# Kernel tuning notes

Hardware: AMD Instinct MI355X
Metric: run time of the kernel (lower is better)

## Reference

```python
import jax, jax.numpy as jnp
import numpy as np
from jax import lax

K = 7            # cfg.network.PSROI_BINS == pool_size
FEAT_STRIDE = 16
LAMDA = 0.1
D_PER_BIN = 8    # feature channels per position-sensitive bin -> C = K*K*8 = 392


def _bilinear(feat, y, x, extra_idx):
    """Bilinearly sample feat[H,W,...] at float coords (y,x); extra_idx are
    integer index arrays (broadcast to y.shape) selecting trailing feat axes."""
    H, W = feat.shape[0], feat.shape[1]
    y0f = jnp.floor(y); x0f = jnp.floor(x)
    wy = (y - y0f)[..., None]
    wx = (x - x0f)[..., None]
    y0 = jnp.clip(y0f.astype(jnp.int32), 0, H - 1)
    y1 = jnp.clip(y0f.astype(jnp.int32) + 1, 0, H - 1)
    x0 = jnp.clip(x0f.astype(jnp.int32), 0, W - 1)
    x1 = jnp.clip(x0f.astype(jnp.int32) + 1, 0, W - 1)
    def g(yi, xi):
        return feat[(yi, xi) + extra_idx]
    return ((1 - wy) * (1 - wx) * g(y0, x0) + (1 - wy) * wx * g(y0, x1)
            + wy * (1 - wx) * g(y1, x0) + wy * wx * g(y1, x1))


def ps_roi(f, rois, k, feat_stride, offsets=None):
    """Position-sensitive RoI pooling. f: [H,W,C] with C = k*k*D (bin-major
    channel layout). rois: [N,5] (batch, x1, y1, x2, y2) in image coords.
    offsets (optional): [N, k*k, G, 2] per-bin, per-channel-group (x,y) shifts
    in image coords. Returns [N, D, k, k]."""
    H, W, C = f.shape
    N = rois.shape[0]
    kk = k * k
    D = C // kk
    x1 = rois[:, 1] / feat_stride
    y1 = rois[:, 2] / feat_stride
    x2 = (rois[:, 3] + 1.0) / feat_stride
    y2 = (rois[:, 4] + 1.0) / feat_stride
    bw = (x2 - x1) / k  # [N]
    bh = (y2 - y1) / k
    jj = jnp.tile(jnp.arange(k, dtype=f.dtype), k)     # bin = i*k + j
    ii = jnp.repeat(jnp.arange(k, dtype=f.dtype), k)
    cx = x1[:, None] + (jj + 0.5) * bw[:, None]        # [N, kk] bin centers
    cy = y1[:, None] + (ii + 0.5) * bh[:, None]
    bins = jnp.arange(kk, dtype=jnp.int32)
    if offsets is None:
        feat = f.reshape(H, W, kk, D)
        b = jnp.broadcast_to(bins, (N, kk))
        vals = _bilinear(feat, cy, cx, (b,))           # [N, kk, D]
    else:
        G = offsets.shape[2]
        cxg = cx[:, :, None] + offsets[..., 0] / feat_stride  # [N, kk, G]
        cyg = cy[:, :, None] + offsets[..., 1] / feat_stride
        feat = f.reshape(H, W, kk, G, D // G)
        b = jnp.broadcast_to(bins[None, :, None], (N, kk, G))
        g = jnp.broadcast_to(jnp.arange(G, dtype=jnp.int32)[None, None, :], (N, kk, G))
        vals = _bilinear(feat, cyg, cxg, (b, g))       # [N, kk, G, D//G]
        vals = vals.reshape(N, kk, D)
    return jnp.transpose(vals.reshape(N, k, k, D), (0, 3, 1, 2))  # [N, D, k, k]


def setup_inputs():
    key = jax.random.key(0)
    kf, kw, k1, k2 = jax.random.split(key, 4)
    H = W = 128
    C = K * K * D_PER_BIN
    N = 2048
    features = jax.random.normal(kf, (1, H, W, C), jnp.float32)
    conv_w = jax.random.normal(kw, (3, 3, C, 2 * 4 * K * K), jnp.float32) * 0.01
    img = float(H * FEAT_STRIDE)
    xy1 = jax.random.uniform(k1, (N, 2), minval=0.0, maxval=img * 0.6)
    wh = jax.random.uniform(k2, (N, 2), minval=32.0, maxval=img * 0.4)
    xy2 = jnp.minimum(xy1 + wh, img - 1.0)
    rois = jnp.concatenate([jnp.zeros((N, 1)), xy1[:, :1], xy1[:, 1:], xy2[:, :1], xy2[:, 1:]], axis=1).astype(jnp.float32)
    return {"features": features, "rois": rois, "conv_w": conv_w}


def reference(features, rois, conv_w):
    # offset branch: 3x3 conv (no bias) -> PS-RoI pool -> scale by lamda*roi size
    offset_map = lax.conv_general_dilated(features, conv_w, (1, 1), 'SAME',
                                          dimension_numbers=('NHWC', 'HWIO', 'NHWC'))
    off = ps_roi(offset_map[0], rois, K, FEAT_STRIDE)          # [N, 8, K, K]
    N = off.shape[0]
    off = off.reshape(N, -1, 2, K, K)                          # [N, 4, 2, K, K]
    off = jnp.transpose(off, (2, 3, 4, 1, 0))                  # [2, K, K, 4, N]
    roi_w = rois[:, 3] - rois[:, 1] + 1.0
    roi_h = rois[:, 4] - rois[:, 2] + 1.0
    off = jnp.stack((off[0] * roi_w * LAMDA, off[1] * roi_h * LAMDA), axis=0)
    off = jnp.transpose(off, (4, 1, 2, 3, 0))                  # [N, K, K, 4, 2]
    off = off.reshape(N, K * K, -1, 2)                         # [N, kk, 4, 2]
    # deformable PS-RoI pooling of the features with predicted offsets
    return ps_roi(features[0], rois, K, FEAT_STRIDE, offsets=off)  # [N, 8, K, K]
```

## Files before the change

### kernel.cpp

```cpp
#include <hip/hip_runtime.h>
#include <cstddef>
#include <cstdint>

#define HH    128
#define WW    128
#define CC    392
#define NPIX  (HH*WW)
#define NROI  2048
#define PSK   7
#define NBIN  49
#define LAMDA 0.1f

#define CPAD      448
#define HPAD      130
#define NPADCO    512
#define SEGSTRIDE (9*CPAD)
#define BKK       64

#define FBM 64
#define FBN 64
#define FBK 32

typedef _Float16 half8   __attribute__((ext_vector_type(8)));
typedef float    floatx4 __attribute__((ext_vector_type(4)));

__device__ __forceinline__ void async_ld16(const _Float16* g, _Float16* l) {
  __builtin_amdgcn_global_load_lds((const __attribute__((address_space(1))) void*)g,
                                   (__attribute__((address_space(3))) void*)l,
                                   16, 0, 0);
}

__global__ __launch_bounds__(256)
void conv_f_kernel(const float* __restrict__ F, _Float16* __restrict__ Fh) {
  const int idx = blockIdx.x * 256 + threadIdx.x;
  const int total = HPAD * HPAD * (CPAD / 8);
  if (idx >= total) return;
  const int p  = idx / (CPAD / 8);
  const int cg = idx - p * (CPAD / 8);
  const int c  = cg * 8;
  const int py = p / HPAD;
  const int px = p - py * HPAD;
  half8 h;
#pragma unroll
  for (int i = 0; i < 8; ++i) h[i] = (_Float16)0.f;
  if (py >= 1 && py <= HH && px >= 1 && px <= WW && c < CC) {
    const float* src = F + ((size_t)(py - 1) * WW + (px - 1)) * CC + c;
    const float4 v0 = *(const float4*)src;
    const float4 v1 = *(const float4*)(src + 4);
    h[0] = (_Float16)v0.x; h[1] = (_Float16)v0.y;
    h[2] = (_Float16)v0.z; h[3] = (_Float16)v0.w;
    h[4] = (_Float16)v1.x; h[5] = (_Float16)v1.y;
    h[6] = (_Float16)v1.z; h[7] = (_Float16)v1.w;
  }
  *(half8*)(Fh + (size_t)p * CPAD + c) = h;
}

__global__ __launch_bounds__(256)
void conv_w_kernel(const float* __restrict__ Wt, _Float16* __restrict__ Bth) {
  __shared__ float tile[32][33];
  const int bid = blockIdx.x;
  const int seg = bid / (14 * 16);
  const int rem = bid - seg * (14 * 16);
  const int cit = rem / 16;
  const int cot = rem - cit * 16;
  const int ci0 = cit * 32, co0 = cot * 32;
  const int t = threadIdx.x;
#pragma unroll
  for (int i = 0; i < 4; ++i) {
    const int idx = t + i * 256;
    const int lr = idx >> 5;
    const int lc = idx & 31;
    const int ci = ci0 + lr, co = co0 + lc;
    float v = 0.f;
    if (ci < CC && co < CC) v = Wt[((size_t)seg * CC + ci) * CC + co];
    tile[lr][lc] = v;
  }
  __syncthreads();
#pragma unroll
  for (int i = 0; i < 4; ++i) {
    const int idx = t + i * 256;
    const int lr = idx >> 5;
    const int lc = idx & 31;
    Bth[(size_t)(co0 + lr) * SEGSTRIDE + seg * CPAD + ci0 + lc] = (_Float16)tile[lc][lr];
  }
}

__global__ __launch_bounds__(256, 2)
void conv_mfma_kernel(const _Float16* __restrict__ Fh, const _Float16* __restrict__ Bth,
                      _Float16* __restrict__ OM) {
  __shared__ __align__(16) _Float16 As[128 * BKK];
  __shared__ __align__(16) _Float16 Bs[128 * BKK];

  const int t = threadIdx.x;
  const int L = t & 63;
  const int w = t >> 6;
  const int row0 = blockIdx.x * 128;
  const int col0 = blockIdx.y * 128;

  const int srow = L >> 3;
  const int kofs = ((L & 7) ^ srow) * 8;

  const int ya = row0 >> 7;
  const int nbase = col0 + w * 32 + srow;

  const int wm = (w >> 1) * 64;
  const int wn = (w & 1) * 64;
  const int fr = L & 15;
  const int quad = L >> 4;
  const int pg0 = (quad ^ (fr & 7)) * 8;
  const int pg1 = ((4 + quad) ^ (fr & 7)) * 8;

  floatx4 acc[4][4];
#pragma unroll
  for (int i = 0; i < 4; ++i)
#pragma unroll
    for (int j = 0; j < 4; ++j) {
      floatx4 z = {0.f, 0.f, 0.f, 0.f};
      acc[i][j] = z;
    }

  for (int seg = 0; seg < 9; ++seg) {
    const int dy = seg / 3 - 1;
    const int dx = seg - (seg / 3) * 3 - 1;
    const int fy = ya + 1 + dy;
    const _Float16* gArow = Fh + ((size_t)fy * HPAD + (1 + dx)) * CPAD + kofs;
    const _Float16* gB = Bth + (size_t)nbase * SEGSTRIDE + seg * CPAD + kofs;

    for (int it = 0; it < 7; ++it) {
      const int cb = it * BKK;
#pragma unroll
      for (int j = 0; j < 4; ++j) {
        const int xr = w * 32 + j * 8 + srow;
        async_ld16(gArow + (size_t)xr * CPAD + cb, &As[(w * 32 + j * 8) * BKK]);
      }
#pragma unroll
      for (int j = 0; j < 4; ++j) {
        async_ld16(gB + (size_t)(j * 8) * SEGSTRIDE + cb, &Bs[(w * 32 + j * 8) * BKK]);
      }
      __syncthreads();

      half8 a0[4], a1[4], b0[4], b1[4];
#pragma unroll
      for (int mt = 0; mt < 4; ++mt) {
        const int rb = (wm + mt * 16 + fr) * BKK;
        a0[mt] = *(const half8*)(&As[rb + pg0]);
        a1[mt] = *(const half8*)(&As[rb + pg1]);
      }
#pragma unroll
      for (int nt = 0; nt < 4; ++nt) {
        const int rb = (wn + nt * 16 + fr) * BKK;
        b0[nt] = *(const half8*)(&Bs[rb + pg0]);
        b1[nt] = *(const half8*)(&Bs[rb + pg1]);
      }
#pragma unroll
      for (int mt = 0; mt < 4; ++mt)
#pragma unroll
        for (int nt = 0; nt < 4; ++nt)
          acc[mt][nt] = __builtin_amdgcn_mfma_f32_16x16x32_f16(a0[mt], b0[nt], acc[mt][nt], 0, 0, 0);
#pragma unroll
      for (int mt = 0; mt < 4; ++mt)
#pragma unroll
        for (int nt = 0; nt < 4; ++nt)
          acc[mt][nt] = __builtin_amdgcn_mfma_f32_16x16x32_f16(a1[mt], b1[nt], acc[mt][nt], 0, 0, 0);
      __syncthreads();
    }
  }

#pragma unroll
  for (int mt = 0; mt < 4; ++mt) {
    const int rbase = row0 + wm + mt * 16 + quad * 4;
#pragma unroll
    for (int nt = 0; nt < 4; ++nt) {
      const int col = col0 + wn + nt * 16 + fr;
      if (col < CC) {
#pragma unroll
        for (int r = 0; r < 4; ++r)
          OM[(size_t)(rbase + r) * CC + col] = (_Float16)acc[mt][nt][r];
      }
    }
  }
}

__global__ __launch_bounds__(256)
void conv3x3_kernel(const float* __restrict__ F, const float* __restrict__ Wt,
                    float* __restrict__ OM) {
  __shared__ float Asf[FBK][FBM + 4];
  __shared__ float Bsf[FBK][FBN + 4];

  const int t = threadIdx.x;
  const int ty = t >> 4;
  const int tx = t & 15;
  const int row0 = blockIdx.x * FBM;
  const int col0 = blockIdx.y * FBN;

  float acc[4][4];
#pragma unroll
  for (int i = 0; i < 4; ++i)
#pragma unroll
    for (int j = 0; j < 4; ++j) acc[i][j] = 0.f;

  for (int kc = 0; kc < 117; ++kc) {
    const int seg   = kc / 13;
    const int cbase = (kc - seg * 13) * FBK;
    const int dy    = seg / 3 - 1;
    const int dx    = seg - (seg / 3) * 3 - 1;

#pragma unroll
    for (int rep = 0; rep < (FBM * FBK) / 256; ++rep) {
      const int idx = t + rep * 256;
      const int r  = idx >> 5;
      const int lk = idx & 31;
      const int m  = row0 + r;
      const int y  = m >> 7, x = m & 127;
      const int yy = y + dy, xx = x + dx;
      const int ci = cbase + lk;
      float v = 0.f;
      if ((unsigned)yy < HH && (unsigned)xx < WW && ci < CC)
        v = F[((size_t)(yy * WW + xx)) * CC + ci];
      Asf[lk][r] = v;
    }
#pragma unroll
    for (int rep = 0; rep < (FBK * FBN) / 256; ++rep) {
      const int idx = t + rep * 256;
      const int lk  = idx >> 6;
      const int nn  = idx & 63;
      const int ci  = cbase + lk;
      const int col = col0 + nn;
      float v = 0.f;
      if (ci < CC && col < CC)
        v = Wt[((size_t)(seg * CC + ci)) * CC + col];
      Bsf[lk][nn] = v;
    }
    __syncthreads();

#pragma unroll
    for (int lk = 0; lk < FBK; ++lk) {
      const float4 a4 = *(const float4*)(&Asf[lk][ty * 4]);
      const float4 b4 = *(const float4*)(&Bsf[lk][tx * 4]);
      const float av[4] = {a4.x, a4.y, a4.z, a4.w};
      const float bv[4] = {b4.x, b4.y, b4.z, b4.w};
#pragma unroll
      for (int i = 0; i < 4; ++i)
#pragma unroll
        for (int j = 0; j < 4; ++j)
          acc[i][j] = fmaf(av[i], bv[j], acc[i][j]);
    }
    __syncthreads();
  }

  const int col = col0 + tx * 4;
  if (col < CC) {
#pragma unroll
    for (int i = 0; i < 4; ++i) {
      float4 v = make_float4(acc[i][0], acc[i][1], acc[i][2], acc[i][3]);
      *(float4*)(&OM[((size_t)(row0 + ty * 4 + i)) * CC + col]) = v;
    }
  }
}

__device__ __forceinline__ void bilin_setup(float y, float x,
                                            int& iy0, int& iy1, int& ix0, int& ix1,
                                            float& w00, float& w01, float& w10, float& w11) {
  const float y0f = floorf(y), x0f = floorf(x);
  const float wy = y - y0f, wx = x - x0f;
  const int a = (int)y0f, b = (int)x0f;
  iy0 = min(max(a, 0), HH - 1);
  iy1 = min(max(a + 1, 0), HH - 1);
  ix0 = min(max(b, 0), WW - 1);
  ix1 = min(max(b + 1, 0), WW - 1);
  w00 = (1.f - wy) * (1.f - wx);
  w01 = (1.f - wy) * wx;
  w10 = wy * (1.f - wx);
  w11 = wy * wx;
}

template <typename TOM>
__global__ __launch_bounds__(256)
void psroi_pool_kernel(const float* __restrict__ F, const float* __restrict__ R,
                       const TOM* __restrict__ OM, float* __restrict__ out) {
  const int tid = blockIdx.x * 256 + threadIdx.x;
  if (tid >= NROI * NBIN * 4) return;
  const int g  = tid & 3;
  const int nb = tid >> 2;
  const int n  = nb / NBIN;
  const int b  = nb - n * NBIN;
  const int bi = b / PSK;
  const int bj = b - bi * PSK;

  const float rx1 = R[n * 5 + 1], ry1 = R[n * 5 + 2];
  const float rx2 = R[n * 5 + 3], ry2 = R[n * 5 + 4];

  const float x1 = rx1 * (1.f / 16.f);
  const float y1 = ry1 * (1.f / 16.f);
  const float x2 = (rx2 + 1.f) * (1.f / 16.f);
  const float y2 = (ry2 + 1.f) * (1.f / 16.f);
  const float bw = (x2 - x1) * (1.f / 7.f);
  const float bh = (y2 - y1) * (1.f / 7.f);
  const float cx = x1 + ((float)bj + 0.5f) * bw;
  const float cy = y1 + ((float)bi + 0.5f) * bh;

  int iy0, iy1, ix0, ix1;
  float w00, w01, w10, w11;
  bilin_setup(cy, cx, iy0, iy1, ix0, ix1, w00, w01, w10, w11);

  const size_t c0 = (size_t)b * 8 + 2 * g;
  const size_t s00 = (size_t)(iy0 * WW + ix0) * CC + c0;
  const size_t s01 = (size_t)(iy0 * WW + ix1) * CC + c0;
  const size_t s10 = (size_t)(iy1 * WW + ix0) * CC + c0;
  const size_t s11 = (size_t)(iy1 * WW + ix1) * CC + c0;

  const float ox = w00 * (float)OM[s00]     + w01 * (float)OM[s01]
                 + w10 * (float)OM[s10]     + w11 * (float)OM[s11];
  const float oy = w00 * (float)OM[s00 + 1] + w01 * (float)OM[s01 + 1]
                 + w10 * (float)OM[s10 + 1] + w11 * (float)OM[s11 + 1];

  const float roiw = rx2 - rx1 + 1.f;
  const float roih = ry2 - ry1 + 1.f;
  const float sx = cx + ox * roiw * (LAMDA / 16.f);
  const float sy = cy + oy * roih * (LAMDA / 16.f);

  int jy0, jy1, jx0, jx1;
  float u00, u01, u10, u11;
  bilin_setup(sy, sx, jy0, jy1, jx0, jx1, u00, u01, u10, u11);

  const float2 q00 = *(const float2*)(F + (size_t)(jy0 * WW + jx0) * CC + c0);
  const float2 q01 = *(const float2*)(F + (size_t)(jy0 * WW + jx1) * CC + c0);
  const float2 q10 = *(const float2*)(F + (size_t)(jy1 * WW + jx0) * CC + c0);
  const float2 q11 = *(const float2*)(F + (size_t)(jy1 * WW + jx1) * CC + c0);

  const float v0 = u00 * q00.x + u01 * q01.x + u10 * q10.x + u11 * q11.x;
  const float v1 = u00 * q00.y + u01 * q01.y + u10 * q10.y + u11 * q11.y;

  out[((size_t)n * 8 + 2 * g + 0) * NBIN + b] = v0;
  out[((size_t)n * 8 + 2 * g + 1) * NBIN + b] = v1;
}

extern "C" void kernel_launch(void* const* d_in, const int* in_sizes, int n_in,
                              void* d_out, int out_size, void* d_ws, size_t ws_size,
                              hipStream_t stream) {
  const float* F  = (const float*)d_in[0];
  const float* R  = (const float*)d_in[1];
  const float* Wt = (const float*)d_in[2];
  float* out = (float*)d_out;

  const size_t omBytes  = (size_t)NPIX * CC * sizeof(_Float16);
  const size_t fhBytes  = (size_t)HPAD * HPAD * CPAD * sizeof(_Float16);
  const size_t bthBytes = (size_t)NPADCO * SEGSTRIDE * sizeof(_Float16);
  const size_t need = omBytes + fhBytes + bthBytes;

  const int totalPool = NROI * NBIN * 4;

  if (ws_size >= need) {
    _Float16* OM  = (_Float16*)d_ws;
    _Float16* Fh  = (_Float16*)((char*)d_ws + omBytes);
    _Float16* Bth = (_Float16*)((char*)d_ws + omBytes + fhBytes);

    const int fTotal = HPAD * HPAD * (CPAD / 8);
    conv_f_kernel<<<(fTotal + 255) / 256, 256, 0, stream>>>(F, Fh);
    conv_w_kernel<<<9 * 14 * 16, 256, 0, stream>>>(Wt, Bth);

    dim3 g(NPIX / 128, NPADCO / 128);
    conv_mfma_kernel<<<g, 256, 0, stream>>>(Fh, Bth, OM);

    psroi_pool_kernel<_Float16><<<(totalPool + 255) / 256, 256, 0, stream>>>(F, R, OM, out);
  } else {
    float* OM = (float*)d_ws;
    dim3 cgrid(NPIX / FBM, (CC + FBN - 1) / FBN);
    conv3x3_kernel<<<cgrid, 256, 0, stream>>>(F, Wt, OM);
    psroi_pool_kernel<float><<<(totalPool + 255) / 256, 256, 0, stream>>>(F, R, OM, out);
  }
}
```

Before: 166.4 us.

## Split conv GEMM K-dimension across two blocks and merge prep kernels

The 3x3 conv GEMM reduction (63 K-steps) is split in two halves via a z grid dimension, with each half writing a separate fp32 partial output map. The pooling kernel then sums the two partials when sampling offsets. The two prep kernels are fused into one launch, and the offset map is now stored in fp32 instead of fp16. This doubles the conv grid from 512 blocks to improve CU occupancy, at the cost of more workspace, twice the output-map write traffic and extra gathers in the pooling kernel.

Result: slower. 171.1 us (+2.8%).

```diff
diff --git a/kernel.cpp b/kernel.cpp
--- a/kernel.cpp
+++ b/kernel.cpp
@@ -16,6 +16,7 @@
 #define NPADCO    512
 #define SEGSTRIDE (9*CPAD)
 #define BKK       64
+#define NQ        63
 
 #define FBM 64
 #define FBN 64
@@ -30,64 +31,67 @@
                                    16, 0, 0);
 }
 
+#define FPREP ((HPAD * HPAD * (CPAD / 8) + 255) / 256)
+#define WPREP (9 * 14 * 16)
+
 __global__ __launch_bounds__(256)
-void conv_f_kernel(const float* __restrict__ F, _Float16* __restrict__ Fh) {
-  const int idx = blockIdx.x * 256 + threadIdx.x;
-  const int total = HPAD * HPAD * (CPAD / 8);
-  if (idx >= total) return;
-  const int p  = idx / (CPAD / 8);
-  const int cg = idx - p * (CPAD / 8);
-  const int c  = cg * 8;
-  const int py = p / HPAD;
-  const int px = p - py * HPAD;
-  half8 h;
-#pragma unroll
-  for (int i = 0; i < 8; ++i) h[i] = (_Float16)0.f;
-  if (py >= 1 && py <= HH && px >= 1 && px <= WW && c < CC) {
-    const float* src = F + ((size_t)(py - 1) * WW + (px - 1)) * CC + c;
-    const float4 v0 = *(const float4*)src;
-    const float4 v1 = *(const float4*)(src + 4);
-    h[0] = (_Float16)v0.x; h[1] = (_Float16)v0.y;
-    h[2] = (_Float16)v0.z; h[3] = (_Float16)v0.w;
-    h[4] = (_Float16)v1.x; h[5] = (_Float16)v1.y;
-    h[6] = (_Float16)v1.z; h[7] = (_Float16)v1.w;
-  }
-  *(half8*)(Fh + (size_t)p * CPAD + c) = h;
-}
-
-__global__ __launch_bounds__(256)
-void conv_w_kernel(const float* __restrict__ Wt, _Float16* __restrict__ Bth) {
+void prep_kernel(const float* __restrict__ F, const float* __restrict__ Wt,
+                 _Float16* __restrict__ Fh, _Float16* __restrict__ Bth) {
   __shared__ float tile[32][33];
-  const int bid = blockIdx.x;
-  const int seg = bid / (14 * 16);
-  const int rem = bid - seg * (14 * 16);
-  const int cit = rem / 16;
-  const int cot = rem - cit * 16;
-  const int ci0 = cit * 32, co0 = cot * 32;
   const int t = threadIdx.x;
-#pragma unroll
-  for (int i = 0; i < 4; ++i) {
-    const int idx = t + i * 256;
-    const int lr = idx >> 5;
-    const int lc = idx & 31;
-    const int ci = ci0 + lr, co = co0 + lc;
-    float v = 0.f;
-    if (ci < CC && co < CC) v = Wt[((size_t)seg * CC + ci) * CC + co];
-    tile[lr][lc] = v;
-  }
-  __syncthreads();
-#pragma unroll
-  for (int i = 0; i < 4; ++i) {
-    const int idx = t + i * 256;
-    const int lr = idx >> 5;
-    const int lc = idx & 31;
-    Bth[(size_t)(co0 + lr) * SEGSTRIDE + seg * CPAD + ci0 + lc] = (_Float16)tile[lc][lr];
+  if (blockIdx.x < FPREP) {
+    const int idx = blockIdx.x * 256 + t;
+    const int total = HPAD * HPAD * (CPAD / 8);
+    if (idx >= total) return;
+    const int p  = idx / (CPAD / 8);
+    const int cg = idx - p * (CPAD / 8);
+    const int c  = cg * 8;
+    const int py = p / HPAD;
+    const int px = p - py * HPAD;
+    half8 h;
+#pragma unroll
+    for (int i = 0; i < 8; ++i) h[i] = (_Float16)0.f;
+    if (py >= 1 && py <= HH && px >= 1 && px <= WW && c < CC) {
+      const float* src = F + ((size_t)(py - 1) * WW + (px - 1)) * CC + c;
+      const float4 v0 = *(const float4*)src;
+      const float4 v1 = *(const float4*)(src + 4);
+      h[0] = (_Float16)v0.x; h[1] = (_Float16)v0.y;
+      h[2] = (_Float16)v0.z; h[3] = (_Float16)v0.w;
+      h[4] = (_Float16)v1.x; h[5] = (_Float16)v1.y;
+      h[6] = (_Float16)v1.z; h[7] = (_Float16)v1.w;
+    }
+    *(half8*)(Fh + (size_t)p * CPAD + c) = h;
+  } else {
+    const int bid = blockIdx.x - FPREP;
+    const int seg = bid / (14 * 16);
+    const int rem = bid - seg * (14 * 16);
+    const int cit = rem / 16;
+    const int cot = rem - cit * 16;
+    const int ci0 = cit * 32, co0 = cot * 32;
+#pragma unroll
+    for (int i = 0; i < 4; ++i) {
+      const int idx = t + i * 256;
+      const int lr = idx >> 5;
+      const int lc = idx & 31;
+      const int ci = ci0 + lr, co = co0 + lc;
+      float v = 0.f;
+      if (ci < CC && co < CC) v = Wt[((size_t)seg * CC + ci) * CC + co];
+      tile[lr][lc] = v;
+    }
+    __syncthreads();
+#pragma unroll
+    for (int i = 0; i < 4; ++i) {
+      const int idx = t + i * 256;
+      const int lr = idx >> 5;
+      const int lc = idx & 31;
+      Bth[(size_t)(co0 + lr) * SEGSTRIDE + seg * CPAD + ci0 + lc] = (_Float16)tile[lc][lr];
+    }
   }
 }
 
 __global__ __launch_bounds__(256, 2)
 void conv_mfma_kernel(const _Float16* __restrict__ Fh, const _Float16* __restrict__ Bth,
-                      _Float16* __restrict__ OM) {
+                      float* __restrict__ OMbase, int span) {
   __shared__ __align__(16) _Float16 As[128 * BKK];
   __shared__ __align__(16) _Float16 Bs[128 * BKK];
 
@@ -96,6 +100,10 @@
   const int w = t >> 6;
   const int row0 = blockIdx.x * 128;
   const int col0 = blockIdx.y * 128;
+  const int kz   = blockIdx.z;
+  const int q0 = kz * span;
+  const int q1 = min(NQ, q0 + span);
+  float* __restrict__ OMp = OMbase + (size_t)kz * NPIX * CC;
 
   const int srow = L >> 3;
   const int kofs = ((L & 7) ^ srow) * 8;
@@ -119,51 +127,51 @@
       acc[i][j] = z;
     }
 
-  for (int seg = 0; seg < 9; ++seg) {
+  for (int q = q0; q < q1; ++q) {
+    const int seg = q / 7;
+    const int it  = q - seg * 7;
     const int dy = seg / 3 - 1;
     const int dx = seg - (seg / 3) * 3 - 1;
     const int fy = ya + 1 + dy;
-    const _Float16* gArow = Fh + ((size_t)fy * HPAD + (1 + dx)) * CPAD + kofs;
-    const _Float16* gB = Bth + (size_t)nbase * SEGSTRIDE + seg * CPAD + kofs;
-
-    for (int it = 0; it < 7; ++it) {
-      const int cb = it * BKK;
-#pragma unroll
-      for (int j = 0; j < 4; ++j) {
-        const int xr = w * 32 + j * 8 + srow;
-        async_ld16(gArow + (size_t)xr * CPAD + cb, &As[(w * 32 + j * 8) * BKK]);
-      }
-#pragma unroll
-      for (int j = 0; j < 4; ++j) {
-        async_ld16(gB + (size_t)(j * 8) * SEGSTRIDE + cb, &Bs[(w * 32 + j * 8) * BKK]);
-      }
-      __syncthreads();
-
-      half8 a0[4], a1[4], b0[4], b1[4];
-#pragma unroll
-      for (int mt = 0; mt < 4; ++mt) {
-        const int rb = (wm + mt * 16 + fr) * BKK;
-        a0[mt] = *(const half8*)(&As[rb + pg0]);
-        a1[mt] = *(const half8*)(&As[rb + pg1]);
-      }
-#pragma unroll
-      for (int nt = 0; nt < 4; ++nt) {
-        const int rb = (wn + nt * 16 + fr) * BKK;
-        b0[nt] = *(const half8*)(&Bs[rb + pg0]);
-        b1[nt] = *(const half8*)(&Bs[rb + pg1]);
-      }
-#pragma unroll
-      for (int mt = 0; mt < 4; ++mt)
-#pragma unroll
-        for (int nt = 0; nt < 4; ++nt)
-          acc[mt][nt] = __builtin_amdgcn_mfma_f32_16x16x32_f16(a0[mt], b0[nt], acc[mt][nt], 0, 0, 0);
-#pragma unroll
-      for (int mt = 0; mt < 4; ++mt)
-#pragma unroll
-        for (int nt = 0; nt < 4; ++nt)
-          acc[mt][nt] = __builtin_amdgcn_mfma_f32_16x16x32_f16(a1[mt], b1[nt], acc[mt][nt], 0, 0, 0);
-      __syncthreads();
-    }
+    const int cb = it * BKK;
+    const _Float16* gArow = Fh + ((size_t)fy * HPAD + (1 + dx)) * CPAD + kofs + cb;
+    const _Float16* gB = Bth + (size_t)nbase * SEGSTRIDE + seg * CPAD + kofs + cb;
+
+#pragma unroll
+    for (int j = 0; j < 4; ++j) {
+      const int xr = w * 32 + j * 8 + srow;
+      async_ld16(gArow + (size_t)xr * CPAD, &As[(w * 32 + j * 8) * BKK]);
+    }
+#pragma unroll
+    for (int j = 0; j < 4; ++j) {
+      async_ld16(gB + (size_t)(j * 8) * SEGSTRIDE, &Bs[(w * 32 + j * 8) * BKK]);
+    }
+    __syncthreads();
+
+    half8 a0[4], a1[4], b0[4], b1[4];
+#pragma unroll
+    for (int mt = 0; mt < 4; ++mt) {
+      const int rb = (wm + mt * 16 + fr) * BKK;
+      a0[mt] = *(const half8*)(&As[rb + pg0]);
+      a1[mt] = *(const half8*)(&As[rb + pg1]);
+    }
+#pragma unroll
+    for (int nt = 0; nt < 4; ++nt) {
+      const int rb = (wn + nt * 16 + fr) * BKK;
+      b0[nt] = *(const half8*)(&Bs[rb + pg0]);
+      b1[nt] = *(const half8*)(&Bs[rb + pg1]);
+    }
+#pragma unroll
+    for (int mt = 0; mt < 4; ++mt)
+#pragma unroll
+      for (int nt = 0; nt < 4; ++nt)
+        acc[mt][nt] = __builtin_amdgcn_mfma_f32_16x16x32_f16(a0[mt], b0[nt], acc[mt][nt], 0, 0, 0);
+#pragma unroll
+    for (int mt = 0; mt < 4; ++mt)
+#pragma unroll
+      for (int nt = 0; nt < 4; ++nt)
+        acc[mt][nt] = __builtin_amdgcn_mfma_f32_16x16x32_f16(a1[mt], b1[nt], acc[mt][nt], 0, 0, 0);
+    __syncthreads();
   }
 
 #pragma unroll
@@ -175,7 +183,7 @@
       if (col < CC) {
 #pragma unroll
         for (int r = 0; r < 4; ++r)
-          OM[(size_t)(rbase + r) * CC + col] = (_Float16)acc[mt][nt][r];
+          OMp[(size_t)(rbase + r) * CC + col] = acc[mt][nt][r];
       }
     }
   }
@@ -274,10 +282,10 @@
   w11 = wy * wx;
 }
 
-template <typename TOM>
 __global__ __launch_bounds__(256)
 void psroi_pool_kernel(const float* __restrict__ F, const float* __restrict__ R,
-                       const TOM* __restrict__ OM, float* __restrict__ out) {
+                       const float* __restrict__ OMa, const float* __restrict__ OMb,
+                       float* __restrict__ out, int dual) {
   const int tid = blockIdx.x * 256 + threadIdx.x;
   if (tid >= NROI * NBIN * 4) return;
   const int g  = tid & 3;
@@ -309,10 +317,22 @@
   const size_t s10 = (size_t)(iy1 * WW + ix0) * CC + c0;
   const size_t s11 = (size_t)(iy1 * WW + ix1) * CC + c0;
 
-  const float ox = w00 * (float)OM[s00]     + w01 * (float)OM[s01]
-                 + w10 * (float)OM[s10]     + w11 * (float)OM[s11];
-  const float oy = w00 * (float)OM[s00 + 1] + w01 * (float)OM[s01 + 1]
-                 + w10 * (float)OM[s10 + 1] + w11 * (float)OM[s11 + 1];
+  float2 m00 = *(const float2*)(OMa + s00);
+  float2 m01 = *(const float2*)(OMa + s01);
+  float2 m10 = *(const float2*)(OMa + s10);
+  float2 m11 = *(const float2*)(OMa + s11);
+  if (dual) {
+    const float2 e00 = *(const float2*)(OMb + s00);
+    const float2 e01 = *(const float2*)(OMb + s01);
+    const float2 e10 = *(const float2*)(OMb + s10);
+    const float2 e11 = *(const float2*)(OMb + s11);
+    m00.x += e00.x; m00.y += e00.y;
+    m01.x += e01.x; m01.y += e01.y;
+    m10.x += e10.x; m10.y += e10.y;
+    m11.x += e11.x; m11.y += e11.y;
+  }
+  const float ox = w00 * m00.x + w01 * m01.x + w10 * m10.x + w11 * m11.x;
+  const float oy = w00 * m00.y + w01 * m01.y + w10 * m10.y + w11 * m11.y;
 
   const float roiw = rx2 - rx1 + 1.f;
   const float roih = ry2 - ry1 + 1.f;
@@ -343,30 +363,37 @@
   const float* Wt = (const float*)d_in[2];
   float* out = (float*)d_out;
 
-  const size_t omBytes  = (size_t)NPIX * CC * sizeof(_Float16);
+  const size_t omBytes  = (size_t)NPIX * CC * sizeof(float);
   const size_t fhBytes  = (size_t)HPAD * HPAD * CPAD * sizeof(_Float16);
   const size_t bthBytes = (size_t)NPADCO * SEGSTRIDE * sizeof(_Float16);
-  const size_t need = omBytes + fhBytes + bthBytes;
+  const size_t needDual   = 2 * omBytes + fhBytes + bthBytes;
+  const size_t needSingle = omBytes + fhBytes + bthBytes;
 
   const int totalPool = NROI * NBIN * 4;
-
-  if (ws_size >= need) {
-    _Float16* OM  = (_Float16*)d_ws;
-    _Float16* Fh  = (_Float16*)((char*)d_ws + omBytes);
-    _Float16* Bth = (_Float16*)((char*)d_ws + omBytes + fhBytes);
-
-    const int fTotal = HPAD * HPAD * (CPAD / 8);
-    conv_f_kernel<<<(fTotal + 255) / 256, 256, 0, stream>>>(F, Fh);
-    conv_w_kernel<<<9 * 14 * 16, 256, 0, stream>>>(Wt, Bth);
-
-    dim3 g(NPIX / 128, NPADCO / 128);
-    conv_mfma_kernel<<<g, 256, 0, stream>>>(Fh, Bth, OM);
-
-    psroi_pool_kernel<_Float16><<<(totalPool + 255) / 256, 256, 0, stream>>>(F, R, OM, out);
+  const int poolGrid = (totalPool + 255) / 256;
+
+  if (ws_size >= needSingle) {
+    const int dual = (ws_size >= needDual) ? 1 : 0;
+    float* OMa = (float*)d_ws;
+    float* OMb = OMa + (size_t)NPIX * CC;
+    _Float16* Fh  = (_Float16*)((char*)d_ws + (dual ? 2 : 1) * omBytes);
+    _Float16* Bth = Fh + (size_t)HPAD * HPAD * CPAD;
+
+    prep_kernel<<<FPREP + WPREP, 256, 0, stream>>>(F, Wt, Fh, Bth);
+
+    if (dual) {
+      dim3 g(NPIX / 128, NPADCO / 128, 2);
+      conv_mfma_kernel<<<g, 256, 0, stream>>>(Fh, Bth, OMa, 32);
+    } else {
+      dim3 g(NPIX / 128, NPADCO / 128, 1);
+      conv_mfma_kernel<<<g, 256, 0, stream>>>(Fh, Bth, OMa, NQ);
+    }
+
+    psroi_pool_kernel<<<poolGrid, 256, 0, stream>>>(F, R, OMa, OMb, out, dual);
   } else {
-    float* OM = (float*)d_ws;
+    float* OMa = (float*)d_ws;
     dim3 cgrid(NPIX / FBM, (CC + FBN - 1) / FBN);
-    conv3x3_kernel<<<cgrid, 256, 0, stream>>>(F, Wt, OM);
-    psroi_pool_kernel<float><<<(totalPool + 255) / 256, 256, 0, stream>>>(F, R, OM, out);
-  }
-}
+    conv3x3_kernel<<<cgrid, 256, 0, stream>>>(F, Wt, OMa);
+    psroi_pool_kernel<<<poolGrid, 256, 0, stream>>>(F, R, OMa, OMa, out, 0);
+  }
+}
```

## Fuse prep, conv and pooling into one cooperative persistent kernel

Applied to the files above, without the earlier changes.

Replaces the four separate launches (feature cast, weight transpose, MFMA conv, PS-RoI pooling) with a single cooperative mega-kernel that uses grid-wide syncs between phases. The conv K-loop is flattened into one 63-step loop, and pooling now reads the padded fp16 feature copy with half2 loads instead of fp32 features. The aim is to remove launch gaps and halve the gather traffic in pooling. The risks are that only 512 of the 1024 blocks do conv work, that grid syncs cost time, and that the change drops the fallback path used when the workspace is too small.

New measurement: 165.9 us. About the same (-0.3%).

```diff
diff --git a/kernel.cpp b/kernel.cpp
--- a/kernel.cpp
+++ b/kernel.cpp
@@ -1,6 +1,9 @@
 #include <hip/hip_runtime.h>
+#include <hip/hip_cooperative_groups.h>
 #include <cstddef>
 #include <cstdint>
+
+namespace cg = cooperative_groups;
 
 #define HH    128
 #define WW    128
@@ -16,12 +19,17 @@
 #define NPADCO    512
 #define SEGSTRIDE (9*CPAD)
 #define BKK       64
-
-#define FBM 64
-#define FBN 64
-#define FBK 32
+#define NQ        63
+
+#define NBLK    1024
+#define NTHR    256
+#define GSTRIDE (NBLK*NTHR)
+#define FTOT    (HPAD*HPAD*(CPAD/8))
+#define WTILES  (9*14*16)
+#define POOLTOT (NROI*NBIN*4)
 
 typedef _Float16 half8   __attribute__((ext_vector_type(8)));
+typedef _Float16 half2v  __attribute__((ext_vector_type(2)));
 typedef float    floatx4 __attribute__((ext_vector_type(4)));
 
 __device__ __forceinline__ void async_ld16(const _Float16* g, _Float16* l) {
@@ -30,72 +38,72 @@
                                    16, 0, 0);
 }
 
-__global__ __launch_bounds__(256)
-void conv_f_kernel(const float* __restrict__ F, _Float16* __restrict__ Fh) {
-  const int idx = blockIdx.x * 256 + threadIdx.x;
-  const int total = HPAD * HPAD * (CPAD / 8);
-  if (idx >= total) return;
-  const int p  = idx / (CPAD / 8);
-  const int cg = idx - p * (CPAD / 8);
-  const int c  = cg * 8;
-  const int py = p / HPAD;
-  const int px = p - py * HPAD;
-  half8 h;
-#pragma unroll
-  for (int i = 0; i < 8; ++i) h[i] = (_Float16)0.f;
-  if (py >= 1 && py <= HH && px >= 1 && px <= WW && c < CC) {
-    const float* src = F + ((size_t)(py - 1) * WW + (px - 1)) * CC + c;
-    const float4 v0 = *(const float4*)src;
-    const float4 v1 = *(const float4*)(src + 4);
-    h[0] = (_Float16)v0.x; h[1] = (_Float16)v0.y;
-    h[2] = (_Float16)v0.z; h[3] = (_Float16)v0.w;
-    h[4] = (_Float16)v1.x; h[5] = (_Float16)v1.y;
-    h[6] = (_Float16)v1.z; h[7] = (_Float16)v1.w;
-  }
-  *(half8*)(Fh + (size_t)p * CPAD + c) = h;
-}
-
-__global__ __launch_bounds__(256)
-void conv_w_kernel(const float* __restrict__ Wt, _Float16* __restrict__ Bth) {
-  __shared__ float tile[32][33];
-  const int bid = blockIdx.x;
-  const int seg = bid / (14 * 16);
-  const int rem = bid - seg * (14 * 16);
-  const int cit = rem / 16;
-  const int cot = rem - cit * 16;
-  const int ci0 = cit * 32, co0 = cot * 32;
-  const int t = threadIdx.x;
-#pragma unroll
-  for (int i = 0; i < 4; ++i) {
-    const int idx = t + i * 256;
-    const int lr = idx >> 5;
-    const int lc = idx & 31;
-    const int ci = ci0 + lr, co = co0 + lc;
-    float v = 0.f;
-    if (ci < CC && co < CC) v = Wt[((size_t)seg * CC + ci) * CC + co];
-    tile[lr][lc] = v;
-  }
-  __syncthreads();
-#pragma unroll
-  for (int i = 0; i < 4; ++i) {
-    const int idx = t + i * 256;
-    const int lr = idx >> 5;
-    const int lc = idx & 31;
-    Bth[(size_t)(co0 + lr) * SEGSTRIDE + seg * CPAD + ci0 + lc] = (_Float16)tile[lc][lr];
-  }
-}
-
-__global__ __launch_bounds__(256, 2)
-void conv_mfma_kernel(const _Float16* __restrict__ Fh, const _Float16* __restrict__ Bth,
-                      _Float16* __restrict__ OM) {
-  __shared__ __align__(16) _Float16 As[128 * BKK];
-  __shared__ __align__(16) _Float16 Bs[128 * BKK];
-
-  const int t = threadIdx.x;
+__device__ __forceinline__ void prep_features(const float* __restrict__ F,
+                                              _Float16* __restrict__ Fh,
+                                              int gtid, int stride) {
+  for (int idx = gtid; idx < FTOT; idx += stride) {
+    const int p  = idx / (CPAD / 8);
+    const int cgi = idx - p * (CPAD / 8);
+    const int c  = cgi * 8;
+    const int py = p / HPAD;
+    const int px = p - py * HPAD;
+    half8 h;
+#pragma unroll
+    for (int i = 0; i < 8; ++i) h[i] = (_Float16)0.f;
+    if (py >= 1 && py <= HH && px >= 1 && px <= WW && c < CC) {
+      const float* src = F + ((size_t)(py - 1) * WW + (px - 1)) * CC + c;
+      const float4 v0 = *(const float4*)src;
+      const float4 v1 = *(const float4*)(src + 4);
+      h[0] = (_Float16)v0.x; h[1] = (_Float16)v0.y;
+      h[2] = (_Float16)v0.z; h[3] = (_Float16)v0.w;
+      h[4] = (_Float16)v1.x; h[5] = (_Float16)v1.y;
+      h[6] = (_Float16)v1.z; h[7] = (_Float16)v1.w;
+    }
+    *(half8*)(Fh + (size_t)p * CPAD + c) = h;
+  }
+}
+
+__device__ __forceinline__ void prep_weights(const float* __restrict__ Wt,
+                                             _Float16* __restrict__ Bth,
+                                             float (*tile)[33],
+                                             int bid, int t, int nblocks) {
+  for (int tl = bid; tl < WTILES; tl += nblocks) {
+    const int seg = tl / (14 * 16);
+    const int rem = tl - seg * (14 * 16);
+    const int cit = rem / 16;
+    const int cot = rem - cit * 16;
+    const int ci0 = cit * 32, co0 = cot * 32;
+    __syncthreads();
+#pragma unroll
+    for (int i = 0; i < 4; ++i) {
+      const int idx = t + i * 256;
+      const int lr = idx >> 5;
+      const int lc = idx & 31;
+      const int ci = ci0 + lr, co = co0 + lc;
+      float v = 0.f;
+      if (ci < CC && co < CC) v = Wt[((size_t)seg * CC + ci) * CC + co];
+      tile[lr][lc] = v;
+    }
+    __syncthreads();
+#pragma unroll
+    for (int i = 0; i < 4; ++i) {
+      const int idx = t + i * 256;
+      const int lr = idx >> 5;
+      const int lc = idx & 31;
+      Bth[(size_t)(co0 + lr) * SEGSTRIDE + seg * CPAD + ci0 + lc] = (_Float16)tile[lc][lr];
+    }
+  }
+}
+
+__device__ __forceinline__ void conv_phase(const _Float16* __restrict__ Fh,
+                                           const _Float16* __restrict__ Bth,
+                                           _Float16* __restrict__ OM,
+                                           _Float16* As, _Float16* Bs,
+                                           int cb, int t) {
   const int L = t & 63;
   const int w = t >> 6;
-  const int row0 = blockIdx.x * 128;
-  const int col0 = blockIdx.y * 128;
+  const int row0 = (cb & 127) * 128;
+  const int col0 = (cb >> 7) * 128;
 
   const int srow = L >> 3;
   const int kofs = ((L & 7) ^ srow) * 8;
@@ -119,51 +127,51 @@
       acc[i][j] = z;
     }
 
-  for (int seg = 0; seg < 9; ++seg) {
+  for (int q = 0; q < NQ; ++q) {
+    const int seg = q / 7;
+    const int it  = q - seg * 7;
     const int dy = seg / 3 - 1;
     const int dx = seg - (seg / 3) * 3 - 1;
     const int fy = ya + 1 + dy;
-    const _Float16* gArow = Fh + ((size_t)fy * HPAD + (1 + dx)) * CPAD + kofs;
-    const _Float16* gB = Bth + (size_t)nbase * SEGSTRIDE + seg * CPAD + kofs;
-
-    for (int it = 0; it < 7; ++it) {
-      const int cb = it * BKK;
-#pragma unroll
-      for (int j = 0; j < 4; ++j) {
-        const int xr = w * 32 + j * 8 + srow;
-        async_ld16(gArow + (size_t)xr * CPAD + cb, &As[(w * 32 + j * 8) * BKK]);
-      }
-#pragma unroll
-      for (int j = 0; j < 4; ++j) {
-        async_ld16(gB + (size_t)(j * 8) * SEGSTRIDE + cb, &Bs[(w * 32 + j * 8) * BKK]);
-      }
-      __syncthreads();
-
-      half8 a0[4], a1[4], b0[4], b1[4];
-#pragma unroll
-      for (int mt = 0; mt < 4; ++mt) {
-        const int rb = (wm + mt * 16 + fr) * BKK;
-        a0[mt] = *(const half8*)(&As[rb + pg0]);
-        a1[mt] = *(const half8*)(&As[rb + pg1]);
-      }
-#pragma unroll
-      for (int nt = 0; nt < 4; ++nt) {
-        const int rb = (wn + nt * 16 + fr) * BKK;
-        b0[nt] = *(const half8*)(&Bs[rb + pg0]);
-        b1[nt] = *(const half8*)(&Bs[rb + pg1]);
-      }
-#pragma unroll
-      for (int mt = 0; mt < 4; ++mt)
-#pragma unroll
-        for (int nt = 0; nt < 4; ++nt)
-          acc[mt][nt] = __builtin_amdgcn_mfma_f32_16x16x32_f16(a0[mt], b0[nt], acc[mt][nt], 0, 0, 0);
-#pragma unroll
-      for (int mt = 0; mt < 4; ++mt)
-#pragma unroll
-        for (int nt = 0; nt < 4; ++nt)
-          acc[mt][nt] = __builtin_amdgcn_mfma_f32_16x16x32_f16(a1[mt], b1[nt], acc[mt][nt], 0, 0, 0);
-      __syncthreads();
-    }
+    const int cbofs = it * BKK;
+    const _Float16* gArow = Fh + ((size_t)fy * HPAD + (1 + dx)) * CPAD + kofs + cbofs;
+    const _Float16* gB = Bth + (size_t)nbase * SEGSTRIDE + seg * CPAD + kofs + cbofs;
+
+#pragma unroll
+    for (int j = 0; j < 4; ++j) {
+      const int xr = w * 32 + j * 8 + srow;
+      async_ld16(gArow + (size_t)xr * CPAD, &As[(w * 32 + j * 8) * BKK]);
+    }
+#pragma unroll
+    for (int j = 0; j < 4; ++j) {
+      async_ld16(gB + (size_t)(j * 8) * SEGSTRIDE, &Bs[(w * 32 + j * 8) * BKK]);
+    }
+    __syncthreads();
+
+    half8 a0[4], a1[4], b0[4], b1[4];
+#pragma unroll
+    for (int mt = 0; mt < 4; ++mt) {
+      const int rb = (wm + mt * 16 + fr) * BKK;
+      a0[mt] = *(const half8*)(&As[rb + pg0]);
+      a1[mt] = *(const half8*)(&As[rb + pg1]);
+    }
+#pragma unroll
+    for (int nt = 0; nt < 4; ++nt) {
+      const int rb = (wn + nt * 16 + fr) * BKK;
+      b0[nt] = *(const half8*)(&Bs[rb + pg0]);
+      b1[nt] = *(const half8*)(&Bs[rb + pg1]);
+    }
+#pragma unroll
+    for (int mt = 0; mt < 4; ++mt)
+#pragma unroll
+      for (int nt = 0; nt < 4; ++nt)
+        acc[mt][nt] = __builtin_amdgcn_mfma_f32_16x16x32_f16(a0[mt], b0[nt], acc[mt][nt], 0, 0, 0);
+#pragma unroll
+    for (int mt = 0; mt < 4; ++mt)
+#pragma unroll
+      for (int nt = 0; nt < 4; ++nt)
+        acc[mt][nt] = __builtin_amdgcn_mfma_f32_16x16x32_f16(a1[mt], b1[nt], acc[mt][nt], 0, 0, 0);
+    __syncthreads();
   }
 
 #pragma unroll
@@ -177,83 +185,6 @@
         for (int r = 0; r < 4; ++r)
           OM[(size_t)(rbase + r) * CC + col] = (_Float16)acc[mt][nt][r];
       }
-    }
-  }
-}
-
-__global__ __launch_bounds__(256)
-void conv3x3_kernel(const float* __restrict__ F, const float* __restrict__ Wt,
-                    float* __restrict__ OM) {
-  __shared__ float Asf[FBK][FBM + 4];
-  __shared__ float Bsf[FBK][FBN + 4];
-
-  const int t = threadIdx.x;
-  const int ty = t >> 4;
-  const int tx = t & 15;
-  const int row0 = blockIdx.x * FBM;
-  const int col0 = blockIdx.y * FBN;
-
-  float acc[4][4];
-#pragma unroll
-  for (int i = 0; i < 4; ++i)
-#pragma unroll
-    for (int j = 0; j < 4; ++j) acc[i][j] = 0.f;
-
-  for (int kc = 0; kc < 117; ++kc) {
-    const int seg   = kc / 13;
-    const int cbase = (kc - seg * 13) * FBK;
-    const int dy    = seg / 3 - 1;
-    const int dx    = seg - (seg / 3) * 3 - 1;
-
-#pragma unroll
-    for (int rep = 0; rep < (FBM * FBK) / 256; ++rep) {
-      const int idx = t + rep * 256;
-      const int r  = idx >> 5;
-      const int lk = idx & 31;
-      const int m  = row0 + r;
-      const int y  = m >> 7, x = m & 127;
-      const int yy = y + dy, xx = x + dx;
-      const int ci = cbase + lk;
-      float v = 0.f;
-      if ((unsigned)yy < HH && (unsigned)xx < WW && ci < CC)
-        v = F[((size_t)(yy * WW + xx)) * CC + ci];
-      Asf[lk][r] = v;
-    }
-#pragma unroll
-    for (int rep = 0; rep < (FBK * FBN) / 256; ++rep) {
-      const int idx = t + rep * 256;
-      const int lk  = idx >> 6;
-      const int nn  = idx & 63;
-      const int ci  = cbase + lk;
-      const int col = col0 + nn;
-      float v = 0.f;
-      if (ci < CC && col < CC)
-        v = Wt[((size_t)(seg * CC + ci)) * CC + col];
-      Bsf[lk][nn] = v;
-    }
-    __syncthreads();
-
-#pragma unroll
-    for (int lk = 0; lk < FBK; ++lk) {
-      const float4 a4 = *(const float4*)(&Asf[lk][ty * 4]);
-      const float4 b4 = *(const float4*)(&Bsf[lk][tx * 4]);
-      const float av[4] = {a4.x, a4.y, a4.z, a4.w};
-      const float bv[4] = {b4.x, b4.y, b4.z, b4.w};
-#pragma unroll
-      for (int i = 0; i < 4; ++i)
-#pragma unroll
-        for (int j = 0; j < 4; ++j)
-          acc[i][j] = fmaf(av[i], bv[j], acc[i][j]);
-    }
-    __syncthreads();
-  }
-
-  const int col = col0 + tx * 4;
-  if (col < CC) {
-#pragma unroll
-    for (int i = 0; i < 4; ++i) {
-      float4 v = make_float4(acc[i][0], acc[i][1], acc[i][2], acc[i][3]);
-      *(float4*)(&OM[((size_t)(row0 + ty * 4 + i)) * CC + col]) = v;
     }
   }
 }
@@ -274,12 +205,10 @@
   w11 = wy * wx;
 }
 
-template <typename TOM>
-__global__ __launch_bounds__(256)
-void psroi_pool_kernel(const float* __restrict__ F, const float* __restrict__ R,
-                       const TOM* __restrict__ OM, float* __restrict__ out) {
-  const int tid = blockIdx.x * 256 + threadIdx.x;
-  if (tid >= NROI * NBIN * 4) return;
+__device__ __forceinline__ void pool_item(const _Float16* __restrict__ Fh,
+                                          const float* __restrict__ R,
+                                          const _Float16* __restrict__ OM,
+                                          float* __restrict__ out, int tid) {
   const int g  = tid & 3;
   const int nb = tid >> 2;
   const int n  = nb / NBIN;
@@ -289,7 +218,6 @@
 
   const float rx1 = R[n * 5 + 1], ry1 = R[n * 5 + 2];
   const float rx2 = R[n * 5 + 3], ry2 = R[n * 5 + 4];
-
   const float x1 = rx1 * (1.f / 16.f);
   const float y1 = ry1 * (1.f / 16.f);
   const float x2 = (rx2 + 1.f) * (1.f / 16.f);
@@ -298,41 +226,94 @@
   const float bh = (y2 - y1) * (1.f / 7.f);
   const float cx = x1 + ((float)bj + 0.5f) * bw;
   const float cy = y1 + ((float)bi + 0.5f) * bh;
+  const float sxs = (rx2 - rx1 + 1.f) * (LAMDA / 16.f);
+  const float sys = (ry2 - ry1 + 1.f) * (LAMDA / 16.f);
 
   int iy0, iy1, ix0, ix1;
   float w00, w01, w10, w11;
   bilin_setup(cy, cx, iy0, iy1, ix0, ix1, w00, w01, w10, w11);
 
   const size_t c0 = (size_t)b * 8 + 2 * g;
-  const size_t s00 = (size_t)(iy0 * WW + ix0) * CC + c0;
-  const size_t s01 = (size_t)(iy0 * WW + ix1) * CC + c0;
-  const size_t s10 = (size_t)(iy1 * WW + ix0) * CC + c0;
-  const size_t s11 = (size_t)(iy1 * WW + ix1) * CC + c0;
-
-  const float ox = w00 * (float)OM[s00]     + w01 * (float)OM[s01]
-                 + w10 * (float)OM[s10]     + w11 * (float)OM[s11];
-  const float oy = w00 * (float)OM[s00 + 1] + w01 * (float)OM[s01 + 1]
-                 + w10 * (float)OM[s10 + 1] + w11 * (float)OM[s11 + 1];
-
-  const float roiw = rx2 - rx1 + 1.f;
-  const float roih = ry2 - ry1 + 1.f;
-  const float sx = cx + ox * roiw * (LAMDA / 16.f);
-  const float sy = cy + oy * roih * (LAMDA / 16.f);
+  const half2v m00 = *(const half2v*)(OM + (size_t)(iy0 * WW + ix0) * CC + c0);
+  const half2v m01 = *(const half2v*)(OM + (size_t)(iy0 * WW + ix1) * CC + c0);
+  const half2v m10 = *(const half2v*)(OM + (size_t)(iy1 * WW + ix0) * CC + c0);
+  const half2v m11 = *(const half2v*)(OM + (size_t)(iy1 * WW + ix1) * CC + c0);
+
+  const float ox = w00 * (float)m00[0] + w01 * (float)m01[0]
+                 + w10 * (float)m10[0] + w11 * (float)m11[0];
+  const float oy = w00 * (float)m00[1] + w01 * (float)m01[1]
+                 + w10 * (float)m10[1] + w11 * (float)m11[1];
+
+  const float sx = cx + ox * sxs;
+  const float sy = cy + oy * sys;
 
   int jy0, jy1, jx0, jx1;
   float u00, u01, u10, u11;
   bilin_setup(sy, sx, jy0, jy1, jx0, jx1, u00, u01, u10, u11);
 
-  const float2 q00 = *(const float2*)(F + (size_t)(jy0 * WW + jx0) * CC + c0);
-  const float2 q01 = *(const float2*)(F + (size_t)(jy0 * WW + jx1) * CC + c0);
-  const float2 q10 = *(const float2*)(F + (size_t)(jy1 * WW + jx0) * CC + c0);
-  const float2 q11 = *(const float2*)(F + (size_t)(jy1 * WW + jx1) * CC + c0);
-
-  const float v0 = u00 * q00.x + u01 * q01.x + u10 * q10.x + u11 * q11.x;
-  const float v1 = u00 * q00.y + u01 * q01.y + u10 * q10.y + u11 * q11.y;
+  const half2v q00 = *(const half2v*)(Fh + ((size_t)(jy0 + 1) * HPAD + (jx0 + 1)) * CPAD + c0);
+  const half2v q01 = *(const half2v*)(Fh + ((size_t)(jy0 + 1) * HPAD + (jx1 + 1)) * CPAD + c0);
+  const half2v q10 = *(const half2v*)(Fh + ((size_t)(jy1 + 1) * HPAD + (jx0 + 1)) * CPAD + c0);
+  const half2v q11 = *(const half2v*)(Fh + ((size_t)(jy1 + 1) * HPAD + (jx1 + 1)) * CPAD + c0);
+
+  const float v0 = u00 * (float)q00[0] + u01 * (float)q01[0]
+                 + u10 * (float)q10[0] + u11 * (float)q11[0];
+  const float v1 = u00 * (float)q00[1] + u01 * (float)q01[1]
+                 + u10 * (float)q10[1] + u11 * (float)q11[1];
 
   out[((size_t)n * 8 + 2 * g + 0) * NBIN + b] = v0;
   out[((size_t)n * 8 + 2 * g + 1) * NBIN + b] = v1;
+}
+
+__global__ __launch_bounds__(NTHR, 4)
+void mega_kernel(const float* __restrict__ F, const float* __restrict__ R,
+                 const float* __restrict__ Wt, _Float16* __restrict__ OM,
+                 _Float16* __restrict__ Fh, _Float16* __restrict__ Bth,
+                 float* __restrict__ out) {
+  __shared__ __align__(16) _Float16 smem[2 * 128 * BKK];
+  const int bid = blockIdx.x;
+  const int t = threadIdx.x;
+  const int gtid = bid * NTHR + t;
+  cg::grid_group grid = cg::this_grid();
+
+  prep_features(F, Fh, gtid, GSTRIDE);
+  prep_weights(Wt, Bth, (float(*)[33])smem, bid, t, NBLK);
+
+  __threadfence();
+  grid.sync();
+
+  if (bid < 512)
+    conv_phase(Fh, Bth, OM, smem, smem + 128 * BKK, bid, t);
+
+  __threadfence();
+  grid.sync();
+
+  for (int item = gtid; item < POOLTOT; item += GSTRIDE)
+    pool_item(Fh, R, OM, out, item);
+}
+
+__global__ __launch_bounds__(256)
+void prep_kernel_sa(const float* __restrict__ F, const float* __restrict__ Wt,
+                    _Float16* __restrict__ Fh, _Float16* __restrict__ Bth) {
+  __shared__ float tile[32][33];
+  const int bid = blockIdx.x;
+  const int t = threadIdx.x;
+  prep_features(F, Fh, bid * 256 + t, gridDim.x * 256);
+  prep_weights(Wt, Bth, tile, bid, t, gridDim.x);
+}
+
+__global__ __launch_bounds__(256, 4)
+void conv_kernel_sa(const _Float16* __restrict__ Fh, const _Float16* __restrict__ Bth,
+                    _Float16* __restrict__ OM) {
+  __shared__ __align__(16) _Float16 smem[2 * 128 * BKK];
+  conv_phase(Fh, Bth, OM, smem, smem + 128 * BKK, blockIdx.x, threadIdx.x);
+}
+
+__global__ __launch_bounds__(256)
+void pool_kernel_sa(const _Float16* __restrict__ Fh, const float* __restrict__ R,
+                    const _Float16* __restrict__ OM, float* __restrict__ out) {
+  const int tid = blockIdx.x * 256 + threadIdx.x;
+  if (tid < POOLTOT) pool_item(Fh, R, OM, out, tid);
 }
 
 extern "C" void kernel_launch(void* const* d_in, const int* in_sizes, int n_in,
@@ -345,28 +326,26 @@
 
   const size_t omBytes  = (size_t)NPIX * CC * sizeof(_Float16);
   const size_t fhBytes  = (size_t)HPAD * HPAD * CPAD * sizeof(_Float16);
-  const size_t bthBytes = (size_t)NPADCO * SEGSTRIDE * sizeof(_Float16);
-  const size_t need = omBytes + fhBytes + bthBytes;
-
-  const int totalPool = NROI * NBIN * 4;
-
-  if (ws_size >= need) {
-    _Float16* OM  = (_Float16*)d_ws;
-    _Float16* Fh  = (_Float16*)((char*)d_ws + omBytes);
-    _Float16* Bth = (_Float16*)((char*)d_ws + omBytes + fhBytes);
-
-    const int fTotal = HPAD * HPAD * (CPAD / 8);
-    conv_f_kernel<<<(fTotal + 255) / 256, 256, 0, stream>>>(F, Fh);
-    conv_w_kernel<<<9 * 14 * 16, 256, 0, stream>>>(Wt, Bth);
-
-    dim3 g(NPIX / 128, NPADCO / 128);
-    conv_mfma_kernel<<<g, 256, 0, stream>>>(Fh, Bth, OM);
-
-    psroi_pool_kernel<_Float16><<<(totalPool + 255) / 256, 256, 0, stream>>>(F, R, OM, out);
-  } else {
-    float* OM = (float*)d_ws;
-    dim3 cgrid(NPIX / FBM, (CC + FBN - 1) / FBN);
-    conv3x3_kernel<<<cgrid, 256, 0, stream>>>(F, Wt, OM);
-    psroi_pool_kernel<float><<<(totalPool + 255) / 256, 256, 0, stream>>>(F, R, OM, out);
-  }
-}
+
+  _Float16* OM  = (_Float16*)d_ws;
+  _Float16* Fh  = (_Float16*)((char*)d_ws + omBytes);
+  _Float16* Bth = (_Float16*)((char*)d_ws + omBytes + fhBytes);
+
+  int maxBlk = 0;
+  hipError_t qerr = hipOccupancyMaxActiveBlocksPerMultiprocessor(&maxBlk, mega_kernel, NTHR, 0);
+  bool tryCoop = (qerr == hipSuccess && maxBlk >= 4);
+
+  if (tryCoop) {
+    void* args[] = {(void*)&F, (void*)&R, (void*)&Wt, (void*)&OM,
+                    (void*)&Fh, (void*)&Bth, (void*)&out};
+    hipError_t err = hipLaunchCooperativeKernel((const void*)mega_kernel,
+                                                dim3(NBLK), dim3(NTHR),
+                                                args, 0, stream);
+    if (err == hipSuccess) return;
+    (void)hipGetLastError();
+  }
+
+  prep_kernel_sa<<<2048, 256, 0, stream>>>(F, Wt, Fh, Bth);
+  conv_kernel_sa<<<512, 256, 0, stream>>>(Fh, Bth, OM);
+  pool_kernel_sa<<<(POOLTOT + 255) / 256, 256, 0, stream>>>(Fh, R, OM, out);
+}
```
